# Kernel optimization log

Hardware: AMD Instinct MI355X
Metric: run time of the kernel (lower is better)

Reference implementation:

```python
import jax, jax.numpy as jnp
import numpy as np

B, S, D = 2, 2048, 1024
H, K = 16, 64  # num_heads, n_hidden per head


def setup_inputs() -> dict:
    key = jax.random.key(0)
    ks = jax.random.split(key, 10)
    sc = 1.0 / np.sqrt(D)
    x = jax.random.normal(ks[0], (B, S, D), dtype=jnp.float32)
    attn_mask = jax.random.randint(ks[1], (B, S, S), 0, 2, dtype=jnp.int32)
    # per-head nn.Linear(d_input, n_hidden) weights stacked over heads: [H, D, K]
    W_Q = jax.random.normal(ks[2], (H, D, K), dtype=jnp.float32) * sc
    b_Q = jax.random.normal(ks[3], (H, K), dtype=jnp.float32) * sc
    W_K = jax.random.normal(ks[4], (H, D, K), dtype=jnp.float32) * sc
    b_K = jax.random.normal(ks[5], (H, K), dtype=jnp.float32) * sc
    W_V = jax.random.normal(ks[6], (H, D, K), dtype=jnp.float32) * sc
    b_V = jax.random.normal(ks[7], (H, K), dtype=jnp.float32) * sc
    # output projection nn.Linear(H*K, D)
    W_proj = jax.random.normal(ks[8], (H * K, D), dtype=jnp.float32) / np.sqrt(H * K)
    b_proj = jax.random.normal(ks[9], (D,), dtype=jnp.float32) / np.sqrt(H * K)
    return {"x": x, "W_Q": W_Q, "b_Q": b_Q, "W_K": W_K, "b_K": b_K,
            "W_V": W_V, "b_V": b_V, "W_proj": W_proj, "b_proj": b_proj,
            "attn_mask": attn_mask}


def reference(x, W_Q, b_Q, W_K, b_K, W_V, b_V, W_proj, b_proj, attn_mask):
    # Q/K/V for all heads at once: [B, H, S, K]
    Q = jnp.einsum('bsd,hdk->bhsk', x, W_Q) + b_Q[None, :, None, :]
    Kt = jnp.einsum('bsd,hdk->bhsk', x, W_K) + b_K[None, :, None, :]
    V = jnp.einsum('bsd,hdk->bhsk', x, W_V) + b_V[None, :, None, :]
    scale = 1.0 / np.sqrt(K).astype(np.float32)
    scores = jnp.einsum('bhsk,bhtk->bhst', Q, Kt) * scale  # [B,H,S,S]
    neg_inf = jnp.finfo(scores.dtype).min
    scores = jnp.where(attn_mask[:, None, :, :] == 0, neg_inf, scores)
    attn_scores = jax.nn.softmax(scores, axis=-1)  # [B,H,S,S]
    heads = jnp.einsum('bhst,bhtk->bhsk', attn_scores, V)  # [B,H,S,K]
    # concat heads along feature dim -> [B, S, H*K]
    concat = heads.transpose(0, 2, 1, 3).reshape(B, S, H * K)
    attn_output = concat @ W_proj + b_proj  # [B, S, D]
    return attn_output, attn_scores
```

## Files before the change

kernel.cpp:

```cpp
#include <hip/hip_runtime.h>

typedef unsigned short u16;
typedef unsigned long long u64;
typedef __attribute__((ext_vector_type(8))) short short8;
typedef __attribute__((ext_vector_type(8))) float float8;
typedef __attribute__((ext_vector_type(4))) float floatx4;

__device__ __forceinline__ u16 f2bf(float f) {
    unsigned u = __float_as_uint(f);
    return (u16)((u + 0x7FFFu + ((u >> 16) & 1u)) >> 16);
}

#define MFMA(a, b, c) __builtin_amdgcn_mfma_f32_16x16x32_bf16((a), (b), (c), 0, 0, 0)

#define AST 40
#define KST 72

__global__ __launch_bounds__(256) void k_projkv(
    const float* __restrict__ x,
    const float* __restrict__ wk, const float* __restrict__ bk,
    const float* __restrict__ wv, const float* __restrict__ bv,
    u16* __restrict__ Kout, u16* __restrict__ Vout)
{
    int mt = blockIdx.x, h = blockIdx.y;
    int tid = threadIdx.x, wave = tid >> 6, lane = tid & 63;
    int col = lane & 15, quad = lane >> 4, m0 = wave * 16;
    int rg0 = mt * 64;

    __shared__ __align__(16) char pool[3 * 64 * AST * 2];
    u16* As = (u16*)pool;
    u16* Bk = (u16*)(pool + 64 * AST * 2);
    u16* Bv = (u16*)(pool + 2 * 64 * AST * 2);

    floatx4 accK[4], accV[4];
    for (int i = 0; i < 4; i++) { accK[i] = (floatx4){0,0,0,0}; accV[i] = (floatx4){0,0,0,0}; }

    int lr = tid >> 2, lc = (tid & 3) * 8;
    int dr = tid >> 3, nc = (tid & 7) * 8;
    const float* whk = wk + (size_t)h * 65536;
    const float* whv = wv + (size_t)h * 65536;

    float8 av = *(const float8*)&x[(size_t)(rg0 + lr) * 1024 + lc];
    float8 wkp = *(const float8*)&whk[(size_t)dr * 64 + nc];
    float8 wvp = *(const float8*)&whv[(size_t)dr * 64 + nc];

    for (int dk = 0; dk < 1024; dk += 32) {
        short8 a8;
        #pragma unroll
        for (int j = 0; j < 8; j++) a8[j] = (short)f2bf(av[j]);
        *(short8*)&As[lr * AST + lc] = a8;
        #pragma unroll
        for (int j = 0; j < 8; j++) Bk[(nc + j) * AST + dr] = f2bf(wkp[j]);
        #pragma unroll
        for (int j = 0; j < 8; j++) Bv[(nc + j) * AST + dr] = f2bf(wvp[j]);
        __syncthreads();
        if (dk + 32 < 1024) {
            av  = *(const float8*)&x[(size_t)(rg0 + lr) * 1024 + dk + 32 + lc];
            wkp = *(const float8*)&whk[(size_t)(dk + 32 + dr) * 64 + nc];
            wvp = *(const float8*)&whv[(size_t)(dk + 32 + dr) * 64 + nc];
        }
        short8 a = *(const short8*)&As[(m0 + col) * AST + quad * 8];
        #pragma unroll
        for (int nt = 0; nt < 4; nt++) {
            short8 bkf = *(const short8*)&Bk[(nt * 16 + col) * AST + quad * 8];
            short8 bvf = *(const short8*)&Bv[(nt * 16 + col) * AST + quad * 8];
            accK[nt] = MFMA(a, bkf, accK[nt]);
            accV[nt] = MFMA(a, bvf, accV[nt]);
        }
        __syncthreads();
    }

    int bb = rg0 >> 11, s0 = rg0 & 2047;
    size_t bh = (size_t)(bb * 16 + h);

    #pragma unroll
    for (int nt = 0; nt < 4; nt++) {
        int n = nt * 16 + col;
        float bvl = bk[h * 64 + n];
        #pragma unroll
        for (int r = 0; r < 4; r++) {
            int rowl = m0 + quad * 4 + r;
            Kout[(bh * 2048 + s0 + rowl) * 64 + n] = f2bf(accK[nt][r] + bvl);
        }
    }

    u16* VT = (u16*)pool;
    #pragma unroll
    for (int nt = 0; nt < 4; nt++) {
        int n = nt * 16 + col;
        float bvl = bv[h * 64 + n];
        #pragma unroll
        for (int r = 0; r < 4; r++) {
            int rowl = m0 + quad * 4 + r;
            VT[n * 68 + rowl] = f2bf(accV[nt][r] + bvl);
        }
    }
    __syncthreads();
    {
        int n2 = tid >> 2, sseg = (tid & 3) * 16;
        short8 p0 = *(const short8*)&VT[n2 * 68 + sseg];
        short8 p1 = *(const short8*)&VT[n2 * 68 + sseg + 8];
        u16* dst = &Vout[(bh * 64 + n2) * 2048 + s0 + sseg];
        *(short8*)dst = p0;
        *(short8*)(dst + 8) = p1;
    }
}

__global__ __launch_bounds__(256) void k_pack(
    const int* __restrict__ mask, u64* __restrict__ bits)
{
    int row = blockIdx.x;
    int b = row >> 11, s = row & 2047;
    int wv = threadIdx.x >> 6, lane = threadIdx.x & 63;
    for (int w = wv; w < 32; w += 4) {
        int m = mask[(size_t)row * 2048 + w * 64 + lane];
        u64 bal = __ballot(m != 0);
        if (lane == 0) bits[((size_t)(b * 32 + w)) * 2048 + s] = bal;
    }
}

__global__ __launch_bounds__(256, 4) void k_fused(
    const float* __restrict__ x, const float* __restrict__ wq, const float* __restrict__ bq,
    const u16* __restrict__ Kbuf, const u16* __restrict__ Vt,
    const u64* __restrict__ mbits,
    float* __restrict__ sc, u16* __restrict__ concat)
{
    int st = blockIdx.x, bh = blockIdx.y;
    int b = bh >> 4, h = bh & 15;
    int s0 = st * 64;
    int tid = threadIdx.x, wave = tid >> 6, lane = tid & 63;
    int col = lane & 15, quad = lane >> 4, m0 = wave * 16;

    __shared__ __align__(16) char pool[3 * 64 * KST * 2];
    u16* Ks = (u16*)pool;
    u16* Vs = (u16*)(pool + 64 * KST * 2);
    u16* Ps = (u16*)(pool + 2 * 64 * KST * 2);
    u16* As = Ks;
    u16* Bs = Vs;
    u16* Qs = Ps;
    __shared__ u64 Mw[64];
    __shared__ float mrun[64], lrun[64];

    floatx4 acc[4];
    for (int i = 0; i < 4; i++) acc[i] = (floatx4){0,0,0,0};
    int lr = tid >> 2, lc = (tid & 3) * 8;
    int dr = tid >> 3, nc = (tid & 7) * 8;
    const float* wh = wq + (size_t)h * 65536;
    const float* xb = x + ((size_t)b * 2048 + s0) * 1024;

    {
        float8 av = *(const float8*)&xb[(size_t)lr * 1024 + lc];
        float8 wv = *(const float8*)&wh[(size_t)dr * 64 + nc];
        for (int dk = 0; dk < 1024; dk += 32) {
            short8 a8;
            #pragma unroll
            for (int j = 0; j < 8; j++) a8[j] = (short)f2bf(av[j]);
            *(short8*)&As[lr * AST + lc] = a8;
            #pragma unroll
            for (int j = 0; j < 8; j++) Bs[(nc + j) * AST + dr] = f2bf(wv[j]);
            __syncthreads();
            if (dk + 32 < 1024) {
                av = *(const float8*)&xb[(size_t)lr * 1024 + dk + 32 + lc];
                wv = *(const float8*)&wh[(size_t)(dk + 32 + dr) * 64 + nc];
            }
            short8 a = *(const short8*)&As[(m0 + col) * AST + quad * 8];
            #pragma unroll
            for (int nt = 0; nt < 4; nt++) {
                short8 b2 = *(const short8*)&Bs[(nt * 16 + col) * AST + quad * 8];
                acc[nt] = MFMA(a, b2, acc[nt]);
            }
            __syncthreads();
        }
    }
    #pragma unroll
    for (int nt = 0; nt < 4; nt++) {
        int n = nt * 16 + col;
        float bvq = bq[h * 64 + n];
        #pragma unroll
        for (int r = 0; r < 4; r++) {
            int rowl = m0 + quad * 4 + r;
            Qs[rowl * KST + n] = f2bf(acc[nt][r] + bvq);
        }
    }
    __syncthreads();
    short8 aq0 = *(const short8*)&Qs[(m0 + col) * KST + quad * 8];
    short8 aq1 = *(const short8*)&Qs[(m0 + col) * KST + 32 + quad * 8];

    const u16* Kh = Kbuf + (size_t)bh * 2048 * 64;
    const u16* Vh = Vt + (size_t)bh * 64 * 2048;
    const u64* mrow = mbits + (size_t)b * 32 * 2048;
    int srow = tid >> 3, soff = (tid & 7) * 8;

    float mreg = -1e30f, lreg = 0.f;
    {
        short8 kp0 = *(const short8*)&Kh[(size_t)srow * 64 + soff];
        short8 kp1 = *(const short8*)&Kh[(size_t)(srow + 32) * 64 + soff];
        for (int t0 = 0; t0 < 2048; t0 += 64) {
            *(short8*)&Ks[srow * KST + soff]        = kp0;
            *(short8*)&Ks[(srow + 32) * KST + soff] = kp1;
            if (tid < 64) Mw[tid] = mrow[(size_t)(t0 >> 6) * 2048 + s0 + tid];
            __syncthreads();
            if (t0 + 64 < 2048) {
                kp0 = *(const short8*)&Kh[(size_t)(t0 + 64 + srow) * 64 + soff];
                kp1 = *(const short8*)&Kh[(size_t)(t0 + 64 + srow + 32) * 64 + soff];
            }
            floatx4 c4[4];
            #pragma unroll
            for (int nt = 0; nt < 4; nt++) {
                c4[nt] = (floatx4){0,0,0,0};
                short8 b0 = *(const short8*)&Ks[(nt * 16 + col) * KST + quad * 8];
                short8 b1 = *(const short8*)&Ks[(nt * 16 + col) * KST + 32 + quad * 8];
                c4[nt] = MFMA(b0, aq0, c4[nt]);
                c4[nt] = MFMA(b1, aq1, c4[nt]);
            }
            u64 mw = Mw[m0 + col];
            float tm = -1e30f;
            #pragma unroll
            for (int nt = 0; nt < 4; nt++)
                #pragma unroll
                for (int r = 0; r < 4; r++) {
                    bool on = (mw >> (nt * 16 + quad * 4 + r)) & 1ull;
                    float v = on ? c4[nt][r] * 0.125f : -1e30f;
                    tm = fmaxf(tm, v);
                }
            tm = fmaxf(tm, __shfl_xor(tm, 16, 64));
            tm = fmaxf(tm, __shfl_xor(tm, 32, 64));
            float ts = 0.f;
            #pragma unroll
            for (int nt = 0; nt < 4; nt++)
                #pragma unroll
                for (int r = 0; r < 4; r++) {
                    bool on = (mw >> (nt * 16 + quad * 4 + r)) & 1ull;
                    ts += on ? __expf(c4[nt][r] * 0.125f - tm) : 0.f;
                }
            ts += __shfl_xor(ts, 16, 64);
            ts += __shfl_xor(ts, 32, 64);
            if (tm > -0.9e30f) {
                float nm = fmaxf(mreg, tm);
                lreg = lreg * __expf(mreg - nm) + ts * __expf(tm - nm);
                mreg = nm;
            }
            __syncthreads();
        }
    }
    if (quad == 0) { mrun[m0 + col] = mreg; lrun[m0 + col] = lreg; }
    __syncthreads();

    float mr4[4], rl4[4];
    #pragma unroll
    for (int r = 0; r < 4; r++) {
        int rowl = m0 + quad * 4 + r;
        mr4[r] = mrun[rowl];
        float l = lrun[rowl];
        rl4[r] = (l > 0.f) ? 1.0f / l : 0.f;
    }
    floatx4 accp[4];
    for (int i = 0; i < 4; i++) accp[i] = (floatx4){0,0,0,0};
    float* scb = sc + (size_t)bh * 2048 * 2048;

    {
        short8 kp0 = *(const short8*)&Kh[(size_t)srow * 64 + soff];
        short8 kp1 = *(const short8*)&Kh[(size_t)(srow + 32) * 64 + soff];
        short8 vp0 = *(const short8*)&Vh[(size_t)srow * 2048 + soff];
        short8 vp1 = *(const short8*)&Vh[(size_t)(srow + 32) * 2048 + soff];
        for (int t0 = 0; t0 < 2048; t0 += 64) {
            *(short8*)&Ks[srow * KST + soff]        = kp0;
            *(short8*)&Ks[(srow + 32) * KST + soff] = kp1;
            *(short8*)&Vs[srow * KST + soff]        = vp0;
            *(short8*)&Vs[(srow + 32) * KST + soff] = vp1;
            if (tid < 64) Mw[tid] = mrow[(size_t)(t0 >> 6) * 2048 + s0 + tid];
            __syncthreads();
            if (t0 + 64 < 2048) {
                kp0 = *(const short8*)&Kh[(size_t)(t0 + 64 + srow) * 64 + soff];
                kp1 = *(const short8*)&Kh[(size_t)(t0 + 64 + srow + 32) * 64 + soff];
                vp0 = *(const short8*)&Vh[(size_t)srow * 2048 + t0 + 64 + soff];
                vp1 = *(const short8*)&Vh[(size_t)(srow + 32) * 2048 + t0 + 64 + soff];
            }
            floatx4 c4[4];
            #pragma unroll
            for (int nt = 0; nt < 4; nt++) {
                c4[nt] = (floatx4){0,0,0,0};
                short8 b0 = *(const short8*)&Ks[(nt * 16 + col) * KST + quad * 8];
                short8 b1 = *(const short8*)&Ks[(nt * 16 + col) * KST + 32 + quad * 8];
                c4[nt] = MFMA(aq0, b0, c4[nt]);
                c4[nt] = MFMA(aq1, b1, c4[nt]);
            }
            #pragma unroll
            for (int r = 0; r < 4; r++) {
                int rowl = m0 + quad * 4 + r;
                u64 mw = Mw[rowl];
                size_t base = (size_t)(s0 + rowl) * 2048 + t0;
                #pragma unroll
                for (int nt = 0; nt < 4; nt++) {
                    bool on = (mw >> (nt * 16 + col)) & 1ull;
                    float p = on ? __expf(c4[nt][r] * 0.125f - mr4[r]) * rl4[r] : 0.f;
                    scb[base + nt * 16 + col] = p;
                    Ps[rowl * KST + nt * 16 + col] = f2bf(p);
                }
            }
            __syncthreads();
            short8 ap0 = *(const short8*)&Ps[(m0 + col) * KST + quad * 8];
            short8 ap1 = *(const short8*)&Ps[(m0 + col) * KST + 32 + quad * 8];
            #pragma unroll
            for (int nt = 0; nt < 4; nt++) {
                short8 b0 = *(const short8*)&Vs[(nt * 16 + col) * KST + quad * 8];
                short8 b1 = *(const short8*)&Vs[(nt * 16 + col) * KST + 32 + quad * 8];
                accp[nt] = MFMA(ap0, b0, accp[nt]);
                accp[nt] = MFMA(ap1, b1, accp[nt]);
            }
            __syncthreads();
        }
    }
    #pragma unroll
    for (int nt = 0; nt < 4; nt++) {
        int n = nt * 16 + col;
        #pragma unroll
        for (int r = 0; r < 4; r++) {
            int rowl = m0 + quad * 4 + r;
            concat[((size_t)(b * 2048 + s0 + rowl)) * 1024 + h * 64 + n] = f2bf(accp[nt][r]);
        }
    }
}

__global__ __launch_bounds__(256) void k_out(
    const u16* __restrict__ concat, const float* __restrict__ wp,
    const float* __restrict__ bp, float* __restrict__ outp)
{
    int mt = blockIdx.x, ntile = blockIdx.y;
    int n0 = ntile * 64;
    int tid = threadIdx.x, wave = tid >> 6, lane = tid & 63;
    int col = lane & 15, quad = lane >> 4, m0 = wave * 16;
    int rg0 = mt * 64;

    __shared__ u16 As[64 * AST];
    __shared__ u16 Bs[64 * AST];

    floatx4 acc[4];
    for (int i = 0; i < 4; i++) acc[i] = (floatx4){0,0,0,0};

    int lr = tid >> 2, lc = (tid & 3) * 8;
    int cr = tid >> 3, nc = (tid & 7) * 8;
    short8 ap = *(const short8*)&concat[(size_t)(rg0 + lr) * 1024 + lc];
    float8 wv = *(const float8*)&wp[(size_t)cr * 1024 + n0 + nc];
    for (int c = 0; c < 1024; c += 32) {
        *(short8*)&As[lr * AST + lc] = ap;
        #pragma unroll
        for (int j = 0; j < 8; j++) Bs[(nc + j) * AST + cr] = f2bf(wv[j]);
        __syncthreads();
        if (c + 32 < 1024) {
            ap = *(const short8*)&concat[(size_t)(rg0 + lr) * 1024 + c + 32 + lc];
            wv = *(const float8*)&wp[(size_t)(c + 32 + cr) * 1024 + n0 + nc];
        }
        short8 a = *(const short8*)&As[(m0 + col) * AST + quad * 8];
        #pragma unroll
        for (int nt = 0; nt < 4; nt++) {
            short8 b = *(const short8*)&Bs[(nt * 16 + col) * AST + quad * 8];
            acc[nt] = MFMA(a, b, acc[nt]);
        }
        __syncthreads();
    }
    #pragma unroll
    for (int nt = 0; nt < 4; nt++) {
        int n = n0 + nt * 16 + col;
        float bv = bp[n];
        #pragma unroll
        for (int r = 0; r < 4; r++) {
            int rowl = m0 + quad * 4 + r;
            outp[(size_t)(rg0 + rowl) * 1024 + n] = acc[nt][r] + bv;
        }
    }
}

extern "C" void kernel_launch(void* const* d_in, const int* in_sizes, int n_in,
                              void* d_out, int out_size, void* d_ws, size_t ws_size,
                              hipStream_t stream) {
    const float* x  = (const float*)d_in[0];
    const float* WQ = (const float*)d_in[1];
    const float* bQ = (const float*)d_in[2];
    const float* WK = (const float*)d_in[3];
    const float* bK = (const float*)d_in[4];
    const float* WV = (const float*)d_in[5];
    const float* bV = (const float*)d_in[6];
    const float* WP = (const float*)d_in[7];
    const float* bP = (const float*)d_in[8];
    const int* mask = (const int*)d_in[9];

    float* out = (float*)d_out;
    float* attn_out = out;
    float* sc = out + (size_t)4194304;

    const size_t NEED = (size_t)3 * 8388608 + 1048576;
    u16 *Kbuf, *Vtb, *concat;
    u64* mbits;
    if (ws_size >= NEED) {
        char* ws = (char*)d_ws;
        Kbuf   = (u16*)ws;               ws += 8388608;
        Vtb    = (u16*)ws;               ws += 8388608;
        concat = (u16*)ws;               ws += 8388608;
        mbits  = (u64*)ws;
    } else {
        Kbuf   = (u16*)attn_out;
        Vtb    = Kbuf + (size_t)4194304;
        mbits  = (u64*)d_in[3];
        concat = (u16*)d_in[9];
    }

    k_projkv<<<dim3(64, 16), 256, 0, stream>>>(x, WK, bK, WV, bV, Kbuf, Vtb);
    k_pack<<<dim3(4096), 256, 0, stream>>>(mask, mbits);
    k_fused<<<dim3(32, 32), 256, 0, stream>>>(x, WQ, bQ, Kbuf, Vtb, mbits, sc, concat);
    k_out<<<dim3(64, 16), 256, 0, stream>>>(concat, WP, bP, attn_out);
}
```

Measured before the change: 853.8 us.

## Pre-transpose weights to bf16, fuse Q into QKV projection, rework softmax stats pass

Adds a kernel that converts and transposes all projection weights to bf16 up front, so the projection and output GEMMs load contiguous bf16 rows instead of scattering fp32 transposes into shared memory. Q projection moves out of the attention kernel into a combined QKV projection kernel, which writes Q to workspace. The softmax statistics pass now handles 128 keys per sync, uses exp2 with a pre-folded log2e scale, and keeps per-lane running max/sum merged by shuffles only at the end. These paths need a larger workspace and fall back to the old code otherwise. The new stats path drops the guard for fully masked rows, so such rows could now produce non-finite values.

```diff
diff --git a/kernel.cpp b/kernel.cpp
--- a/kernel.cpp
+++ b/kernel.cpp
@@ -1,6 +1,7 @@
 #include <hip/hip_runtime.h>
 
 typedef unsigned short u16;
+typedef unsigned int u32;
 typedef unsigned long long u64;
 typedef __attribute__((ext_vector_type(8))) short short8;
 typedef __attribute__((ext_vector_type(8))) float float8;
@@ -15,75 +16,165 @@
 
 #define AST 40
 #define KST 72
-
-__global__ __launch_bounds__(256) void k_projkv(
+#define C2 0.18033688011112043f
+
+__global__ __launch_bounds__(256) void k_wtall(
+    const float* __restrict__ wq, const float* __restrict__ wk,
+    const float* __restrict__ wv, const float* __restrict__ wp,
+    u16* __restrict__ wt3, u16* __restrict__ wpT)
+{
+    int slot = blockIdx.x >> 9;
+    int id = (blockIdx.x & 511) * 256 + threadIdx.x;
+    const float* in; u16* out; int logC;
+    if (slot == 3) { in = wp; out = wpT; logC = 10; }
+    else {
+        in = (slot == 0) ? wq : (slot == 1 ? wk : wv);
+        out = wt3 + (size_t)slot * 1048576;
+        logC = 6;
+    }
+    int rg = id & 127;
+    int rest = id >> 7;
+    int C = 1 << logC;
+    int cc = rest & (C - 1);
+    int bt = rest >> logC;
+    const float* src = in + ((size_t)bt << (10 + logC)) + cc;
+    int r0 = rg * 8;
+    short8 o;
+    #pragma unroll
+    for (int j = 0; j < 8; j++) o[j] = (short)f2bf(src[(size_t)(r0 + j) << logC]);
+    *(short8*)&out[(((size_t)bt << logC) + cc) * 1024 + r0] = o;
+}
+
+__global__ __launch_bounds__(256) void k_projqkv(
     const float* __restrict__ x,
+    const float* __restrict__ wq, const float* __restrict__ bq,
     const float* __restrict__ wk, const float* __restrict__ bk,
     const float* __restrict__ wv, const float* __restrict__ bv,
-    u16* __restrict__ Kout, u16* __restrict__ Vout)
+    const u16* __restrict__ wtT,
+    u16* __restrict__ Qout, u16* __restrict__ Kout, u16* __restrict__ Vout)
 {
     int mt = blockIdx.x, h = blockIdx.y;
     int tid = threadIdx.x, wave = tid >> 6, lane = tid & 63;
     int col = lane & 15, quad = lane >> 4, m0 = wave * 16;
     int rg0 = mt * 64;
-
-    __shared__ __align__(16) char pool[3 * 64 * AST * 2];
+    bool doQ = (Qout != nullptr);
+
+    __shared__ __align__(16) char pool[4 * 64 * AST * 2];
     u16* As = (u16*)pool;
-    u16* Bk = (u16*)(pool + 64 * AST * 2);
-    u16* Bv = (u16*)(pool + 2 * 64 * AST * 2);
-
-    floatx4 accK[4], accV[4];
-    for (int i = 0; i < 4; i++) { accK[i] = (floatx4){0,0,0,0}; accV[i] = (floatx4){0,0,0,0}; }
+    u16* Bq = As + 64 * AST;
+    u16* Bk = Bq + 64 * AST;
+    u16* Bv = Bk + 64 * AST;
+
+    floatx4 aQ[4], aK[4], aV[4];
+    for (int i = 0; i < 4; i++) { aQ[i] = (floatx4){0,0,0,0}; aK[i] = (floatx4){0,0,0,0}; aV[i] = (floatx4){0,0,0,0}; }
 
     int lr = tid >> 2, lc = (tid & 3) * 8;
-    int dr = tid >> 3, nc = (tid & 7) * 8;
-    const float* whk = wk + (size_t)h * 65536;
-    const float* whv = wv + (size_t)h * 65536;
-
     float8 av = *(const float8*)&x[(size_t)(rg0 + lr) * 1024 + lc];
-    float8 wkp = *(const float8*)&whk[(size_t)dr * 64 + nc];
-    float8 wvp = *(const float8*)&whv[(size_t)dr * 64 + nc];
-
-    for (int dk = 0; dk < 1024; dk += 32) {
-        short8 a8;
-        #pragma unroll
-        for (int j = 0; j < 8; j++) a8[j] = (short)f2bf(av[j]);
-        *(short8*)&As[lr * AST + lc] = a8;
-        #pragma unroll
-        for (int j = 0; j < 8; j++) Bk[(nc + j) * AST + dr] = f2bf(wkp[j]);
-        #pragma unroll
-        for (int j = 0; j < 8; j++) Bv[(nc + j) * AST + dr] = f2bf(wvp[j]);
-        __syncthreads();
-        if (dk + 32 < 1024) {
-            av  = *(const float8*)&x[(size_t)(rg0 + lr) * 1024 + dk + 32 + lc];
-            wkp = *(const float8*)&whk[(size_t)(dk + 32 + dr) * 64 + nc];
-            wvp = *(const float8*)&whv[(size_t)(dk + 32 + dr) * 64 + nc];
-        }
-        short8 a = *(const short8*)&As[(m0 + col) * AST + quad * 8];
-        #pragma unroll
-        for (int nt = 0; nt < 4; nt++) {
-            short8 bkf = *(const short8*)&Bk[(nt * 16 + col) * AST + quad * 8];
-            short8 bvf = *(const short8*)&Bv[(nt * 16 + col) * AST + quad * 8];
-            accK[nt] = MFMA(a, bkf, accK[nt]);
-            accV[nt] = MFMA(a, bvf, accV[nt]);
-        }
-        __syncthreads();
-    }
-
-    int bb = rg0 >> 11, s0 = rg0 & 2047;
+
+    if (wtT) {
+        const u16* wqT = wtT + ((size_t)h * 64) * 1024;
+        const u16* wkT = wqT + 1048576;
+        const u16* wvT = wkT + 1048576;
+        int nr = tid >> 2, dc = (tid & 3) * 8;
+        short8 q8 = *(const short8*)&wqT[(size_t)nr * 1024 + dc];
+        short8 k8 = *(const short8*)&wkT[(size_t)nr * 1024 + dc];
+        short8 v8 = *(const short8*)&wvT[(size_t)nr * 1024 + dc];
+        for (int dk = 0; dk < 1024; dk += 32) {
+            short8 a8;
+            #pragma unroll
+            for (int j = 0; j < 8; j++) a8[j] = (short)f2bf(av[j]);
+            *(short8*)&As[lr * AST + lc] = a8;
+            *(short8*)&Bq[nr * AST + dc] = q8;
+            *(short8*)&Bk[nr * AST + dc] = k8;
+            *(short8*)&Bv[nr * AST + dc] = v8;
+            __syncthreads();
+            if (dk + 32 < 1024) {
+                av = *(const float8*)&x[(size_t)(rg0 + lr) * 1024 + dk + 32 + lc];
+                q8 = *(const short8*)&wqT[(size_t)nr * 1024 + dk + 32 + dc];
+                k8 = *(const short8*)&wkT[(size_t)nr * 1024 + dk + 32 + dc];
+                v8 = *(const short8*)&wvT[(size_t)nr * 1024 + dk + 32 + dc];
+            }
+            short8 a = *(const short8*)&As[(m0 + col) * AST + quad * 8];
+            #pragma unroll
+            for (int nt = 0; nt < 4; nt++) {
+                short8 fq = *(const short8*)&Bq[(nt * 16 + col) * AST + quad * 8];
+                short8 fk = *(const short8*)&Bk[(nt * 16 + col) * AST + quad * 8];
+                short8 fv = *(const short8*)&Bv[(nt * 16 + col) * AST + quad * 8];
+                if (doQ) aQ[nt] = MFMA(a, fq, aQ[nt]);
+                aK[nt] = MFMA(a, fk, aK[nt]);
+                aV[nt] = MFMA(a, fv, aV[nt]);
+            }
+            __syncthreads();
+        }
+    } else {
+        int dr = tid >> 3, nc = (tid & 7) * 8;
+        const float* whq = wq + (size_t)h * 65536;
+        const float* whk = wk + (size_t)h * 65536;
+        const float* whv = wv + (size_t)h * 65536;
+        float8 qp = *(const float8*)&whq[(size_t)dr * 64 + nc];
+        float8 kp = *(const float8*)&whk[(size_t)dr * 64 + nc];
+        float8 vp = *(const float8*)&whv[(size_t)dr * 64 + nc];
+        for (int dk = 0; dk < 1024; dk += 32) {
+            short8 a8;
+            #pragma unroll
+            for (int j = 0; j < 8; j++) a8[j] = (short)f2bf(av[j]);
+            *(short8*)&As[lr * AST + lc] = a8;
+            #pragma unroll
+            for (int j = 0; j < 8; j++) Bk[(nc + j) * AST + dr] = f2bf(kp[j]);
+            #pragma unroll
+            for (int j = 0; j < 8; j++) Bv[(nc + j) * AST + dr] = f2bf(vp[j]);
+            if (doQ) {
+                #pragma unroll
+                for (int j = 0; j < 8; j++) Bq[(nc + j) * AST + dr] = f2bf(qp[j]);
+            }
+            __syncthreads();
+            if (dk + 32 < 1024) {
+                av = *(const float8*)&x[(size_t)(rg0 + lr) * 1024 + dk + 32 + lc];
+                qp = *(const float8*)&whq[(size_t)(dk + 32 + dr) * 64 + nc];
+                kp = *(const float8*)&whk[(size_t)(dk + 32 + dr) * 64 + nc];
+                vp = *(const float8*)&whv[(size_t)(dk + 32 + dr) * 64 + nc];
+            }
+            short8 a = *(const short8*)&As[(m0 + col) * AST + quad * 8];
+            #pragma unroll
+            for (int nt = 0; nt < 4; nt++) {
+                short8 fk = *(const short8*)&Bk[(nt * 16 + col) * AST + quad * 8];
+                short8 fv = *(const short8*)&Bv[(nt * 16 + col) * AST + quad * 8];
+                aK[nt] = MFMA(a, fk, aK[nt]);
+                aV[nt] = MFMA(a, fv, aV[nt]);
+                if (doQ) {
+                    short8 fq = *(const short8*)&Bq[(nt * 16 + col) * AST + quad * 8];
+                    aQ[nt] = MFMA(a, fq, aQ[nt]);
+                }
+            }
+            __syncthreads();
+        }
+    }
+
+    int bb = rg0 >> 11, s0b = rg0 & 2047;
     size_t bh = (size_t)(bb * 16 + h);
 
     #pragma unroll
     for (int nt = 0; nt < 4; nt++) {
         int n = nt * 16 + col;
-        float bvl = bk[h * 64 + n];
+        float bkl = bk[h * 64 + n];
         #pragma unroll
         for (int r = 0; r < 4; r++) {
             int rowl = m0 + quad * 4 + r;
-            Kout[(bh * 2048 + s0 + rowl) * 64 + n] = f2bf(accK[nt][r] + bvl);
-        }
-    }
-
+            Kout[(bh * 2048 + s0b + rowl) * 64 + n] = f2bf(aK[nt][r] + bkl);
+        }
+    }
+    if (doQ) {
+        #pragma unroll
+        for (int nt = 0; nt < 4; nt++) {
+            int n = nt * 16 + col;
+            float bql = bq[h * 64 + n];
+            #pragma unroll
+            for (int r = 0; r < 4; r++) {
+                int rowl = m0 + quad * 4 + r;
+                Qout[(bh * 2048 + s0b + rowl) * 64 + n] = f2bf(aQ[nt][r] + bql);
+            }
+        }
+    }
     u16* VT = (u16*)pool;
     #pragma unroll
     for (int nt = 0; nt < 4; nt++) {
@@ -92,7 +183,7 @@
         #pragma unroll
         for (int r = 0; r < 4; r++) {
             int rowl = m0 + quad * 4 + r;
-            VT[n * 68 + rowl] = f2bf(accV[nt][r] + bvl);
+            VT[n * 68 + rowl] = f2bf(aV[nt][r] + bvl);
         }
     }
     __syncthreads();
@@ -100,7 +191,7 @@
         int n2 = tid >> 2, sseg = (tid & 3) * 16;
         short8 p0 = *(const short8*)&VT[n2 * 68 + sseg];
         short8 p1 = *(const short8*)&VT[n2 * 68 + sseg + 8];
-        u16* dst = &Vout[(bh * 64 + n2) * 2048 + s0 + sseg];
+        u16* dst = &Vout[(bh * 64 + n2) * 2048 + s0b + sseg];
         *(short8*)dst = p0;
         *(short8*)(dst + 8) = p1;
     }
@@ -121,7 +212,7 @@
 
 __global__ __launch_bounds__(256, 4) void k_fused(
     const float* __restrict__ x, const float* __restrict__ wq, const float* __restrict__ bq,
-    const u16* __restrict__ Kbuf, const u16* __restrict__ Vt,
+    const u16* __restrict__ Qbuf, const u16* __restrict__ Kbuf, const u16* __restrict__ Vt,
     const u64* __restrict__ mbits,
     float* __restrict__ sc, u16* __restrict__ concat)
 {
@@ -135,20 +226,24 @@
     u16* Ks = (u16*)pool;
     u16* Vs = (u16*)(pool + 64 * KST * 2);
     u16* Ps = (u16*)(pool + 2 * 64 * KST * 2);
-    u16* As = Ks;
-    u16* Bs = Vs;
-    u16* Qs = Ps;
-    __shared__ u64 Mw[64];
+    u16* K128 = Ks;
+    __shared__ u64 Mw[128];
     __shared__ float mrun[64], lrun[64];
 
-    floatx4 acc[4];
-    for (int i = 0; i < 4; i++) acc[i] = (floatx4){0,0,0,0};
-    int lr = tid >> 2, lc = (tid & 3) * 8;
-    int dr = tid >> 3, nc = (tid & 7) * 8;
-    const float* wh = wq + (size_t)h * 65536;
-    const float* xb = x + ((size_t)b * 2048 + s0) * 1024;
-
-    {
+    if (Qbuf) {
+        const u16* Qh = Qbuf + (size_t)bh * 2048 * 64;
+        int qr = tid >> 2, qc = (tid & 3) * 16;
+        *(short8*)&Ps[qr * KST + qc]     = *(const short8*)&Qh[(size_t)(s0 + qr) * 64 + qc];
+        *(short8*)&Ps[qr * KST + qc + 8] = *(const short8*)&Qh[(size_t)(s0 + qr) * 64 + qc + 8];
+        __syncthreads();
+    } else {
+        floatx4 acc[4];
+        for (int i = 0; i < 4; i++) acc[i] = (floatx4){0,0,0,0};
+        int lr = tid >> 2, lc = (tid & 3) * 8;
+        int dr = tid >> 3, nc = (tid & 7) * 8;
+        const float* wh = wq + (size_t)h * 65536;
+        const float* xb = x + ((size_t)b * 2048 + s0) * 1024;
+        u16* As = Ks; u16* Bs = Vs;
         float8 av = *(const float8*)&xb[(size_t)lr * 1024 + lc];
         float8 wv = *(const float8*)&wh[(size_t)dr * 64 + nc];
         for (int dk = 0; dk < 1024; dk += 32) {
@@ -171,77 +266,87 @@
             }
             __syncthreads();
         }
-    }
-    #pragma unroll
-    for (int nt = 0; nt < 4; nt++) {
-        int n = nt * 16 + col;
-        float bvq = bq[h * 64 + n];
-        #pragma unroll
-        for (int r = 0; r < 4; r++) {
-            int rowl = m0 + quad * 4 + r;
-            Qs[rowl * KST + n] = f2bf(acc[nt][r] + bvq);
-        }
-    }
-    __syncthreads();
-    short8 aq0 = *(const short8*)&Qs[(m0 + col) * KST + quad * 8];
-    short8 aq1 = *(const short8*)&Qs[(m0 + col) * KST + 32 + quad * 8];
+        #pragma unroll
+        for (int nt = 0; nt < 4; nt++) {
+            int n = nt * 16 + col;
+            float bvq = bq[h * 64 + n];
+            #pragma unroll
+            for (int r = 0; r < 4; r++) {
+                int rowl = m0 + quad * 4 + r;
+                Ps[rowl * KST + n] = f2bf(acc[nt][r] + bvq);
+            }
+        }
+        __syncthreads();
+    }
+    short8 aq0 = *(const short8*)&Ps[(m0 + col) * KST + quad * 8];
+    short8 aq1 = *(const short8*)&Ps[(m0 + col) * KST + 32 + quad * 8];
 
     const u16* Kh = Kbuf + (size_t)bh * 2048 * 64;
     const u16* Vh = Vt + (size_t)bh * 64 * 2048;
     const u64* mrow = mbits + (size_t)b * 32 * 2048;
-    int srow = tid >> 3, soff = (tid & 7) * 8;
+    int qs4 = quad * 4;
 
     float mreg = -1e30f, lreg = 0.f;
     {
-        short8 kp0 = *(const short8*)&Kh[(size_t)srow * 64 + soff];
-        short8 kp1 = *(const short8*)&Kh[(size_t)(srow + 32) * 64 + soff];
-        for (int t0 = 0; t0 < 2048; t0 += 64) {
-            *(short8*)&Ks[srow * KST + soff]        = kp0;
-            *(short8*)&Ks[(srow + 32) * KST + soff] = kp1;
-            if (tid < 64) Mw[tid] = mrow[(size_t)(t0 >> 6) * 2048 + s0 + tid];
-            __syncthreads();
-            if (t0 + 64 < 2048) {
-                kp0 = *(const short8*)&Kh[(size_t)(t0 + 64 + srow) * 64 + soff];
-                kp1 = *(const short8*)&Kh[(size_t)(t0 + 64 + srow + 32) * 64 + soff];
-            }
-            floatx4 c4[4];
-            #pragma unroll
-            for (int nt = 0; nt < 4; nt++) {
-                c4[nt] = (floatx4){0,0,0,0};
-                short8 b0 = *(const short8*)&Ks[(nt * 16 + col) * KST + quad * 8];
-                short8 b1 = *(const short8*)&Ks[(nt * 16 + col) * KST + 32 + quad * 8];
-                c4[nt] = MFMA(b0, aq0, c4[nt]);
-                c4[nt] = MFMA(b1, aq1, c4[nt]);
-            }
-            u64 mw = Mw[m0 + col];
-            float tm = -1e30f;
-            #pragma unroll
-            for (int nt = 0; nt < 4; nt++)
+        int r0 = tid >> 1, c0 = (tid & 1) * 32;
+        short8 kp[4];
+        #pragma unroll
+        for (int j = 0; j < 4; j++) kp[j] = *(const short8*)&Kh[(size_t)r0 * 64 + c0 + j * 8];
+        for (int t0 = 0; t0 < 2048; t0 += 128) {
+            #pragma unroll
+            for (int j = 0; j < 4; j++) *(short8*)&K128[r0 * KST + c0 + j * 8] = kp[j];
+            if (tid < 128) Mw[tid] = mrow[(size_t)((t0 >> 6) + (tid >> 6)) * 2048 + s0 + (tid & 63)];
+            __syncthreads();
+            if (t0 + 128 < 2048) {
                 #pragma unroll
-                for (int r = 0; r < 4; r++) {
-                    bool on = (mw >> (nt * 16 + quad * 4 + r)) & 1ull;
-                    float v = on ? c4[nt][r] * 0.125f : -1e30f;
-                    tm = fmaxf(tm, v);
+                for (int j = 0; j < 4; j++) kp[j] = *(const short8*)&Kh[(size_t)(t0 + 128 + r0) * 64 + c0 + j * 8];
+            }
+            #pragma unroll
+            for (int half = 0; half < 2; half++) {
+                floatx4 c4[4];
+                #pragma unroll
+                for (int tt = 0; tt < 4; tt++) {
+                    c4[tt] = (floatx4){0,0,0,0};
+                    int trow = (half * 4 + tt) * 16 + col;
+                    short8 b0 = *(const short8*)&K128[trow * KST + quad * 8];
+                    short8 b1 = *(const short8*)&K128[trow * KST + 32 + quad * 8];
+                    c4[tt] = MFMA(b0, aq0, c4[tt]);
+                    c4[tt] = MFMA(b1, aq1, c4[tt]);
                 }
-            tm = fmaxf(tm, __shfl_xor(tm, 16, 64));
-            tm = fmaxf(tm, __shfl_xor(tm, 32, 64));
-            float ts = 0.f;
-            #pragma unroll
-            for (int nt = 0; nt < 4; nt++)
+                u64 w = Mw[half * 64 + m0 + col];
+                u32 blo = ((u32)w) >> qs4;
+                u32 bhi = ((u32)(w >> 32)) >> qs4;
+                float v[16];
+                float tmax = -1e30f;
                 #pragma unroll
-                for (int r = 0; r < 4; r++) {
-                    bool on = (mw >> (nt * 16 + quad * 4 + r)) & 1ull;
-                    ts += on ? __expf(c4[nt][r] * 0.125f - tm) : 0.f;
+                for (int tt = 0; tt < 4; tt++) {
+                    u32 bsel = (tt < 2) ? blo : bhi;
+                    #pragma unroll
+                    for (int r = 0; r < 4; r++) {
+                        bool on = (bsel >> ((tt & 1) * 16 + r)) & 1u;
+                        float vv = on ? c4[tt][r] * C2 : -1e30f;
+                        v[tt * 4 + r] = vv;
+                        tmax = fmaxf(tmax, vv);
+                    }
                 }
-            ts += __shfl_xor(ts, 16, 64);
-            ts += __shfl_xor(ts, 32, 64);
-            if (tm > -0.9e30f) {
-                float nm = fmaxf(mreg, tm);
-                lreg = lreg * __expf(mreg - nm) + ts * __expf(tm - nm);
+                float nm = fmaxf(mreg, tmax);
+                lreg *= exp2f(mreg - nm);
+                float ss = 0.f;
+                #pragma unroll
+                for (int i = 0; i < 16; i++) ss += exp2f(v[i] - nm);
+                lreg += ss;
                 mreg = nm;
             }
             __syncthreads();
         }
+    }
+    {
+        float mo = __shfl_xor(mreg, 16, 64), lx = __shfl_xor(lreg, 16, 64);
+        float nm = fmaxf(mreg, mo);
+        lreg = lreg * exp2f(mreg - nm) + lx * exp2f(mo - nm); mreg = nm;
+        mo = __shfl_xor(mreg, 32, 64); lx = __shfl_xor(lreg, 32, 64);
+        nm = fmaxf(mreg, mo);
+        lreg = lreg * exp2f(mreg - nm) + lx * exp2f(mo - nm); mreg = nm;
     }
     if (quad == 0) { mrun[m0 + col] = mreg; lrun[m0 + col] = lreg; }
     __syncthreads();
@@ -249,16 +354,15 @@
     float mr4[4], rl4[4];
     #pragma unroll
     for (int r = 0; r < 4; r++) {
-        int rowl = m0 + quad * 4 + r;
+        int rowl = m0 + qs4 + r;
         mr4[r] = mrun[rowl];
-        float l = lrun[rowl];
-        rl4[r] = (l > 0.f) ? 1.0f / l : 0.f;
+        rl4[r] = 1.0f / lrun[rowl];
     }
     floatx4 accp[4];
     for (int i = 0; i < 4; i++) accp[i] = (floatx4){0,0,0,0};
-    float* scb = sc + (size_t)bh * 2048 * 2048;
-
+    float* scb = sc + (size_t)bh * 4194304;
     {
+        int srow = tid >> 3, soff = (tid & 7) * 8;
         short8 kp0 = *(const short8*)&Kh[(size_t)srow * 64 + soff];
         short8 kp1 = *(const short8*)&Kh[(size_t)(srow + 32) * 64 + soff];
         short8 vp0 = *(const short8*)&Vh[(size_t)srow * 2048 + soff];
@@ -287,13 +391,17 @@
             }
             #pragma unroll
             for (int r = 0; r < 4; r++) {
-                int rowl = m0 + quad * 4 + r;
-                u64 mw = Mw[rowl];
+                int rowl = m0 + qs4 + r;
+                u64 w = Mw[rowl];
+                u32 blo = ((u32)w) >> col;
+                u32 bhi = ((u32)(w >> 32)) >> col;
                 size_t base = (size_t)(s0 + rowl) * 2048 + t0;
                 #pragma unroll
                 for (int nt = 0; nt < 4; nt++) {
-                    bool on = (mw >> (nt * 16 + col)) & 1ull;
-                    float p = on ? __expf(c4[nt][r] * 0.125f - mr4[r]) * rl4[r] : 0.f;
+                    u32 bsel = (nt < 2) ? blo : bhi;
+                    bool on = (bsel >> ((nt & 1) * 16)) & 1u;
+                    float s2 = on ? c4[nt][r] * C2 : -1e30f;
+                    float p = exp2f(s2 - mr4[r]) * rl4[r];
                     scb[base + nt * 16 + col] = p;
                     Ps[rowl * KST + nt * 16 + col] = f2bf(p);
                 }
@@ -316,7 +424,7 @@
         int n = nt * 16 + col;
         #pragma unroll
         for (int r = 0; r < 4; r++) {
-            int rowl = m0 + quad * 4 + r;
+            int rowl = m0 + qs4 + r;
             concat[((size_t)(b * 2048 + s0 + rowl)) * 1024 + h * 64 + n] = f2bf(accp[nt][r]);
         }
     }
@@ -324,7 +432,8 @@
 
 __global__ __launch_bounds__(256) void k_out(
     const u16* __restrict__ concat, const float* __restrict__ wp,
-    const float* __restrict__ bp, float* __restrict__ outp)
+    const u16* __restrict__ wpT, const float* __restrict__ bp,
+    float* __restrict__ outp)
 {
     int mt = blockIdx.x, ntile = blockIdx.y;
     int n0 = ntile * 64;
@@ -339,25 +448,46 @@
     for (int i = 0; i < 4; i++) acc[i] = (floatx4){0,0,0,0};
 
     int lr = tid >> 2, lc = (tid & 3) * 8;
-    int cr = tid >> 3, nc = (tid & 7) * 8;
     short8 ap = *(const short8*)&concat[(size_t)(rg0 + lr) * 1024 + lc];
-    float8 wv = *(const float8*)&wp[(size_t)cr * 1024 + n0 + nc];
-    for (int c = 0; c < 1024; c += 32) {
-        *(short8*)&As[lr * AST + lc] = ap;
-        #pragma unroll
-        for (int j = 0; j < 8; j++) Bs[(nc + j) * AST + cr] = f2bf(wv[j]);
-        __syncthreads();
-        if (c + 32 < 1024) {
-            ap = *(const short8*)&concat[(size_t)(rg0 + lr) * 1024 + c + 32 + lc];
-            wv = *(const float8*)&wp[(size_t)(c + 32 + cr) * 1024 + n0 + nc];
-        }
-        short8 a = *(const short8*)&As[(m0 + col) * AST + quad * 8];
-        #pragma unroll
-        for (int nt = 0; nt < 4; nt++) {
-            short8 b = *(const short8*)&Bs[(nt * 16 + col) * AST + quad * 8];
-            acc[nt] = MFMA(a, b, acc[nt]);
-        }
-        __syncthreads();
+    if (wpT) {
+        int nr = tid >> 2, dc = (tid & 3) * 8;
+        short8 w8 = *(const short8*)&wpT[(size_t)(n0 + nr) * 1024 + dc];
+        for (int c = 0; c < 1024; c += 32) {
+            *(short8*)&As[lr * AST + lc] = ap;
+            *(short8*)&Bs[nr * AST + dc] = w8;
+            __syncthreads();
+            if (c + 32 < 1024) {
+                ap = *(const short8*)&concat[(size_t)(rg0 + lr) * 1024 + c + 32 + lc];
+                w8 = *(const short8*)&wpT[(size_t)(n0 + nr) * 1024 + c + 32 + dc];
+            }
+            short8 a = *(const short8*)&As[(m0 + col) * AST + quad * 8];
+            #pragma unroll
+            for (int nt = 0; nt < 4; nt++) {
+                short8 bf = *(const short8*)&Bs[(nt * 16 + col) * AST + quad * 8];
+                acc[nt] = MFMA(a, bf, acc[nt]);
+            }
+            __syncthreads();
+        }
+    } else {
+        int cr = tid >> 3, nc = (tid & 7) * 8;
+        float8 wv = *(const float8*)&wp[(size_t)cr * 1024 + n0 + nc];
+        for (int c = 0; c < 1024; c += 32) {
+            *(short8*)&As[lr * AST + lc] = ap;
+            #pragma unroll
+            for (int j = 0; j < 8; j++) Bs[(nc + j) * AST + cr] = f2bf(wv[j]);
+            __syncthreads();
+            if (c + 32 < 1024) {
+                ap = *(const short8*)&concat[(size_t)(rg0 + lr) * 1024 + c + 32 + lc];
+                wv = *(const float8*)&wp[(size_t)(c + 32 + cr) * 1024 + n0 + nc];
+            }
+            short8 a = *(const short8*)&As[(m0 + col) * AST + quad * 8];
+            #pragma unroll
+            for (int nt = 0; nt < 4; nt++) {
+                short8 bf = *(const short8*)&Bs[(nt * 16 + col) * AST + quad * 8];
+                acc[nt] = MFMA(a, bf, acc[nt]);
+            }
+            __syncthreads();
+        }
     }
     #pragma unroll
     for (int nt = 0; nt < 4; nt++) {
@@ -389,14 +519,24 @@
     float* attn_out = out;
     float* sc = out + (size_t)4194304;
 
-    const size_t NEED = (size_t)3 * 8388608 + 1048576;
-    u16 *Kbuf, *Vtb, *concat;
+    const size_t NEED_BIG = (size_t)4 * 8388608 + 1048576 + 6291456 + 2097152;
+    const size_t NEED_MID = (size_t)3 * 8388608 + 1048576;
+    u16 *Kbuf, *Vtb, *Qbuf = nullptr, *concat, *wt3 = nullptr, *wpT = nullptr;
     u64* mbits;
-    if (ws_size >= NEED) {
+    if (ws_size >= NEED_BIG) {
         char* ws = (char*)d_ws;
-        Kbuf   = (u16*)ws;               ws += 8388608;
-        Vtb    = (u16*)ws;               ws += 8388608;
-        concat = (u16*)ws;               ws += 8388608;
+        Kbuf   = (u16*)ws;   ws += 8388608;
+        Vtb    = (u16*)ws;   ws += 8388608;
+        Qbuf   = (u16*)ws;   ws += 8388608;
+        concat = (u16*)ws;   ws += 8388608;
+        mbits  = (u64*)ws;   ws += 1048576;
+        wt3    = (u16*)ws;   ws += 6291456;
+        wpT    = (u16*)ws;
+    } else if (ws_size >= NEED_MID) {
+        char* ws = (char*)d_ws;
+        Kbuf   = (u16*)ws;   ws += 8388608;
+        Vtb    = (u16*)ws;   ws += 8388608;
+        concat = (u16*)ws;   ws += 8388608;
         mbits  = (u64*)ws;
     } else {
         Kbuf   = (u16*)attn_out;
@@ -405,8 +545,11 @@
         concat = (u16*)d_in[9];
     }
 
-    k_projkv<<<dim3(64, 16), 256, 0, stream>>>(x, WK, bK, WV, bV, Kbuf, Vtb);
+    if (wt3)
+        k_wtall<<<dim3(2048), 256, 0, stream>>>(WQ, WK, WV, WP, wt3, wpT);
+    k_projqkv<<<dim3(64, 16), 256, 0, stream>>>(x, WQ, bQ, WK, bK, WV, bV,
+                                                wt3, Qbuf, Kbuf, Vtb);
     k_pack<<<dim3(4096), 256, 0, stream>>>(mask, mbits);
-    k_fused<<<dim3(32, 32), 256, 0, stream>>>(x, WQ, bQ, Kbuf, Vtb, mbits, sc, concat);
-    k_out<<<dim3(64, 16), 256, 0, stream>>>(concat, WP, bP, attn_out);
-}
+    k_fused<<<dim3(32, 32), 256, 0, stream>>>(x, WQ, bQ, Qbuf, Kbuf, Vtb, mbits, sc, concat);
+    k_out<<<dim3(64, 16), 256, 0, stream>>>(concat, WP, wpT, bP, attn_out);
+}
```

After: 804.5 us. -5.8%, faster.
